# Kernel optimization log

Measured on AMD Instinct MI355X. Metric: run time of the kernel, lower is better.

## Reference

```python
import jax, jax.numpy as jnp
import numpy as np

# GPT-2 decoder (mlm=False path of the Keras GPT module), no past/KV-cache,
# no explicit mask -> causal mask, dropout disabled (training=False).
N_HEAD = 12
NINF = -10000.0  # Attention.ninf
EPS = 1e-6


def layer_norm(x, g, b):
    m = jnp.mean(x, axis=-1, keepdims=True)
    v = jnp.mean(jnp.square(x - m), axis=-1, keepdims=True)
    return (x - m) / jnp.sqrt(v + EPS) * g + b


def gelu(x):
    # 0.5*x*(1+erf(x/sqrt(2))) as in gelu_activating
    return 0.5 * x * (1.0 + jax.lax.erf(x * np.float32(1.0 / np.sqrt(2.0))))


def setup_inputs() -> dict:
    key = jax.random.key(0)
    B, S, D, L, V, CTX = 4, 512, 768, 12, 50257, 1024
    F = 4 * D
    ks = jax.random.split(key, 10)
    init = lambda k, shape: (jax.random.normal(k, shape, jnp.float32) * 0.02)
    return {
        "x": jax.random.randint(ks[0], (B, S), 0, V),
        "emb": init(ks[1], (V, D)),        # wte (tied output projection)
        "posemb": init(ks[2], (CTX, D)),   # wpe
        "ln1_g": jnp.ones((L, D)), "ln1_b": jnp.zeros((L, D)),
        "wqkv": init(ks[3], (L, D, 3 * D)), "bqkv": jnp.zeros((L, 3 * D)),
        "wo": init(ks[4], (L, D, D)), "bo": jnp.zeros((L, D)),
        "ln2_g": jnp.ones((L, D)), "ln2_b": jnp.zeros((L, D)),
        "wfc": init(ks[5], (L, D, F)), "bfc": jnp.zeros((L, F)),
        "wproj": init(ks[6], (L, F, D)), "bproj": jnp.zeros((L, D)),
        "lnf_g": jnp.ones((D,)), "lnf_b": jnp.zeros((D,)),
    }


def reference(x, emb, posemb, ln1_g, ln1_b, wqkv, bqkv, wo, bo,
              ln2_g, ln2_b, wfc, bfc, wproj, bproj, lnf_g, lnf_b):
    B, S = x.shape
    L, D, _ = wqkv.shape
    H = N_HEAD
    hd = D // H
    scale = np.float32(1.0 / np.sqrt(hd))

    # Embedding (mlm=False): token + positional, no layernorm
    h = emb[x] + posemb[:S]  # [B,S,D]

    # causal mask: positions j > i get NINF (m1 = range(q)[:,None] < range(k)-k+q)
    mask = (jnp.arange(S)[:, None] < jnp.arange(S)[None, :]).astype(jnp.float32) * NINF

    for i in range(L):
        # pre-norm attention
        qkv = layer_norm(h, ln1_g[i], ln1_b[i]) @ wqkv[i] + bqkv[i]  # [B,S,3D]
        q, k, v = jnp.split(qkv, 3, axis=-1)
        q = q.reshape(B, S, H, hd).transpose(0, 2, 1, 3)  # [B,H,S,hd]
        k = k.reshape(B, S, H, hd).transpose(0, 2, 1, 3)
        v = v.reshape(B, S, H, hd).transpose(0, 2, 1, 3)
        scores = jnp.einsum('bhqd,bhkd->bhqk', q, k) * scale + mask
        a = jax.nn.softmax(scores, axis=-1)  # [B,H,S,S]
        o = jnp.einsum('bhqk,bhkd->bhqd', a, v)
        o = o.transpose(0, 2, 1, 3).reshape(B, S, D)
        h = h + (o @ wo[i] + bo[i])  # residual
        # pre-norm MLP
        m = layer_norm(h, ln2_g[i], ln2_b[i])
        h = h + (gelu(m @ wfc[i] + bfc[i]) @ wproj[i] + bproj[i])

    hidden = layer_norm(h, lnf_g, lnf_b)          # model/lnorm_f
    logits = hidden @ emb.T                        # tied embedding projection
    probs = jax.nn.softmax(logits, axis=-1)        # softmax=True
    return (probs, hidden)
```

## Files before the change

### kernel.cpp

```cpp
#include <hip/hip_runtime.h>
#include <hip/hip_bf16.h>

typedef __bf16 bf16_t;
typedef bf16_t bf16x8 __attribute__((ext_vector_type(8)));
typedef float  f32x4  __attribute__((ext_vector_type(4)));

__device__ __forceinline__ void gload16(const void* g, void* l) {
    __builtin_amdgcn_global_load_lds(
        (const __attribute__((address_space(1))) unsigned int*)g,
        (__attribute__((address_space(3))) unsigned int*)l, 16, 0, 0);
}

__device__ __forceinline__ void drain_and_barrier() {
    __builtin_amdgcn_sched_barrier(0);
    asm volatile("s_waitcnt vmcnt(0)" ::: "memory");
    __builtin_amdgcn_s_barrier();
    __builtin_amdgcn_sched_barrier(0);
}

__global__ void embed_kernel(const int* __restrict__ x,
                             const float* __restrict__ emb,
                             const float* __restrict__ pos,
                             float* __restrict__ h,
                             int S, int D, int total)
{
    int i = blockIdx.x * blockDim.x + threadIdx.x;
    if (i >= total) return;
    int d  = i % D;
    int bs = i / D;
    int s  = bs % S;
    h[i] = emb[(long long)x[bs] * D + d] + pos[(long long)s * D + d];
}

__global__ void convert_bf16(const float* __restrict__ in, bf16_t* __restrict__ out, int n4)
{
    int i = blockIdx.x * blockDim.x + threadIdx.x;
    for (; i < n4; i += gridDim.x * blockDim.x) {
        float4 v = ((const float4*)in)[i];
        bf16_t* o = out + (size_t)i * 4;
        o[0] = (bf16_t)v.x; o[1] = (bf16_t)v.y; o[2] = (bf16_t)v.z; o[3] = (bf16_t)v.w;
    }
}

__global__ __launch_bounds__(256) void transpose_to_bf16(
    const float* __restrict__ in, bf16_t* __restrict__ out, int K, int N)
{
    const float* ip = in  + (size_t)blockIdx.z * K * N;
    bf16_t*      op = out + (size_t)blockIdx.z * K * N;
    __shared__ float t[32][33];
    const int n0 = blockIdx.x * 32, k0 = blockIdx.y * 32;
    const int tx = threadIdx.x, ty = threadIdx.y;
#pragma unroll
    for (int u = 0; u < 4; ++u)
        t[ty + u * 8][tx] = ip[(size_t)(k0 + ty + u * 8) * N + (n0 + tx)];
    __syncthreads();
#pragma unroll
    for (int u = 0; u < 4; ++u)
        op[(size_t)(n0 + ty + u * 8) * K + (k0 + tx)] = (bf16_t)t[tx][ty + u * 8];
}

__global__ __launch_bounds__(256) void layernorm_dual(
    const float* __restrict__ X, const float* __restrict__ g,
    const float* __restrict__ b, bf16_t* __restrict__ Yb,
    float* __restrict__ Yf, int D)
{
    const int row = blockIdx.x;
    const float* xr = X + (long long)row * D;
    const int tid = threadIdx.x;

    float vals[3];
    float s = 0.0f;
#pragma unroll
    for (int u = 0; u < 3; ++u) { vals[u] = xr[tid + u * 256]; s += vals[u]; }

    __shared__ float red[256];
    red[tid] = s;
    __syncthreads();
    for (int off = 128; off > 0; off >>= 1) {
        if (tid < off) red[tid] += red[tid + off];
        __syncthreads();
    }
    const float mean = red[0] / (float)D;
    __syncthreads();

    float vs = 0.0f;
#pragma unroll
    for (int u = 0; u < 3; ++u) { float d = vals[u] - mean; vs += d * d; }
    red[tid] = vs;
    __syncthreads();
    for (int off = 128; off > 0; off >>= 1) {
        if (tid < off) red[tid] += red[tid + off];
        __syncthreads();
    }
    const float var  = red[0] / (float)D;
    const float rstd = rsqrtf(var + 1e-6f);

#pragma unroll
    for (int u = 0; u < 3; ++u) {
        const int c = tid + u * 256;
        const float y = (vals[u] - mean) * rstd * g[c] + b[c];
        Yb[(long long)row * D + c] = (bf16_t)y;
        if (Yf) Yf[(long long)row * D + c] = y;
    }
}

__global__ __launch_bounds__(256) void flash_attn(
    const bf16_t* __restrict__ qkv, bf16_t* __restrict__ o)
{
    constexpr int S = 512, TD = 2304, D = 768, H = 12;
    const int qt = blockIdx.x;
    const int z  = blockIdx.y;
    const int bb = z / H, hh = z - bb * H;
    const int tid = threadIdx.x, lane = tid & 63, w = tid >> 6;
    const int fr = lane & 15, g = lane >> 4, sub = g * 8;

    __shared__ bf16_t kS[2][4096];
    __shared__ bf16_t vS[2][4096];
    __shared__ bf16_t pS[4][32 * 72];

    bf16x8 qf[2][2];
    const bf16_t* qbase = qkv + (size_t)(bb * S + qt * 128 + w * 32) * TD + hh * 64;
#pragma unroll
    for (int m = 0; m < 2; ++m)
#pragma unroll
        for (int ks = 0; ks < 2; ++ks) {
            bf16x8 v = *(const bf16x8*)&qbase[(size_t)(m * 16 + fr) * TD + ks * 32 + sub];
#pragma unroll
            for (int j = 0; j < 8; ++j) v[j] = v[j] * (bf16_t)0.125f;
            qf[m][ks] = v;
        }

    f32x4 oacc[2][4];
    float mrun[2][4], lrun[2][4];
#pragma unroll
    for (int m = 0; m < 2; ++m)
#pragma unroll
        for (int r = 0; r < 4; ++r) { mrun[m][r] = -3.0e38f; lrun[m][r] = 0.0f; }
#pragma unroll
    for (int m = 0; m < 2; ++m)
#pragma unroll
        for (int n = 0; n < 4; ++n)
            oacc[m][n] = (f32x4){0.f, 0.f, 0.f, 0.f};

    int qr[2][4];
#pragma unroll
    for (int m = 0; m < 2; ++m)
#pragma unroll
        for (int r = 0; r < 4; ++r)
            qr[m][r] = qt * 128 + w * 32 + m * 16 + g * 4 + r;

    const int srow8  = lane >> 3;
    const int schunk = (lane & 7) ^ (srow8 & 7);

    const bf16_t* kGbase = qkv + (size_t)(bb * S) * TD + D + hh * 64;
    const bf16_t* vGbase = qkv + (size_t)(bb * S) * TD + 2 * D + hh * 64;
    const int nkv = 2 * qt + 2;

    bf16x8 vreg[2];

#define STAGE_ISSUE(buf, t)                                                     \
    {                                                                           \
        _Pragma("unroll")                                                       \
        for (int it = 0; it < 2; ++it) {                                        \
            const int row = it * 32 + w * 8 + srow8;                            \
            gload16(kGbase + (size_t)((t) * 64 + row) * TD + schunk * 8,        \
                    &kS[buf][it * 2048 + w * 512]);                             \
        }                                                                       \
        _Pragma("unroll")                                                       \
        for (int it = 0; it < 2; ++it) {                                        \
            const int dch = w * 2 + it;                                         \
            vreg[it] = *(const bf16x8*)&vGbase[(size_t)((t) * 64 + lane) * TD + dch * 8]; \
        }                                                                       \
    }
#define STAGE_WRITE(buf)                                                        \
    {                                                                           \
        _Pragma("unroll")                                                       \
        for (int it = 0; it < 2; ++it) {                                        \
            const int dch = w * 2 + it;                                         \
            _Pragma("unroll")                                                   \
            for (int j = 0; j < 8; ++j) {                                       \
                const int d = dch * 8 + j;                                      \
                vS[buf][d * 64 + (((lane >> 3) ^ j) << 3) + (lane & 7)] = vreg[it][j]; \
            }                                                                   \
        }                                                                       \
    }

    STAGE_ISSUE(0, 0);
    STAGE_WRITE(0);
    __syncthreads();

    int cur = 0;
    for (int t = 0; t < nkv; ++t) {
        if (t + 1 < nkv) STAGE_ISSUE(cur ^ 1, t + 1);

        f32x4 sacc[2][4];
#pragma unroll
        for (int m = 0; m < 2; ++m)
#pragma unroll
            for (int n = 0; n < 4; ++n)
                sacc[m][n] = (f32x4){0.f, 0.f, 0.f, 0.f};
#pragma unroll
        for (int ks = 0; ks < 2; ++ks) {
            bf16x8 bK[4];
#pragma unroll
            for (int n = 0; n < 4; ++n) {
                const int rw = n * 16 + fr;
                const int c  = ks * 4 + g;
                bK[n] = *(const bf16x8*)&kS[cur][rw * 64 + ((c ^ (rw & 7)) << 3)];
            }
#pragma unroll
            for (int m = 0; m < 2; ++m)
#pragma unroll
                for (int n = 0; n < 4; ++n)
                    sacc[m][n] = __builtin_amdgcn_mfma_f32_16x16x32_bf16(
                        qf[m][ks], bK[n], sacc[m][n], 0, 0, 0);
        }

        if (t >= 2 * qt) {
#pragma unroll
            for (int m = 0; m < 2; ++m)
#pragma unroll
                for (int n = 0; n < 4; ++n) {
                    const int key = t * 64 + n * 16 + fr;
#pragma unroll
                    for (int r = 0; r < 4; ++r)
                        if (key > qr[m][r]) sacc[m][n][r] = -3.0e38f;
                }
        }

        float sf[2][4], rs[2][4];
#pragma unroll
        for (int m = 0; m < 2; ++m)
#pragma unroll
            for (int r = 0; r < 4; ++r) {
                float v = fmaxf(fmaxf(sacc[m][0][r], sacc[m][1][r]),
                                fmaxf(sacc[m][2][r], sacc[m][3][r]));
#pragma unroll
                for (int off = 1; off < 16; off <<= 1)
                    v = fmaxf(v, __shfl_xor(v, off));
                const float mn = fmaxf(mrun[m][r], v);
                sf[m][r] = __expf(mrun[m][r] - mn);
                mrun[m][r] = mn;
                lrun[m][r] *= sf[m][r];
            }
#pragma unroll
        for (int m = 0; m < 2; ++m)
#pragma unroll
            for (int n = 0; n < 4; ++n)
#pragma unroll
                for (int r = 0; r < 4; ++r)
                    oacc[m][n][r] *= sf[m][r];
#pragma unroll
        for (int m = 0; m < 2; ++m)
#pragma unroll
            for (int r = 0; r < 4; ++r) rs[m][r] = 0.0f;
#pragma unroll
        for (int m = 0; m < 2; ++m)
#pragma unroll
            for (int n = 0; n < 4; ++n)
#pragma unroll
                for (int r = 0; r < 4; ++r) {
                    const float p = __expf(sacc[m][n][r] - mrun[m][r]);
                    sacc[m][n][r] = p;
                    rs[m][r] += p;
                }
#pragma unroll
        for (int m = 0; m < 2; ++m)
#pragma unroll
            for (int r = 0; r < 4; ++r) {
                float v = rs[m][r];
#pragma unroll
                for (int off = 1; off < 16; off <<= 1) v += __shfl_xor(v, off);
                lrun[m][r] += v;
            }

        bf16_t* pw = pS[w];
#pragma unroll
        for (int m = 0; m < 2; ++m)
#pragma unroll
            for (int n = 0; n < 4; ++n)
#pragma unroll
                for (int r = 0; r < 4; ++r)
                    pw[(m * 16 + g * 4 + r) * 72 + n * 16 + fr] = (bf16_t)sacc[m][n][r];

#pragma unroll
        for (int ks = 0; ks < 2; ++ks) {
            bf16x8 pa[2], vb[4];
#pragma unroll
            for (int m = 0; m < 2; ++m)
                pa[m] = *(const bf16x8*)&pw[(m * 16 + fr) * 72 + ks * 32 + sub];
#pragma unroll
            for (int n = 0; n < 4; ++n) {
                const int rw = n * 16 + fr;
                const int c  = ks * 4 + g;
                vb[n] = *(const bf16x8*)&vS[cur][rw * 64 + ((c ^ (rw & 7)) << 3)];
            }
#pragma unroll
            for (int m = 0; m < 2; ++m)
#pragma unroll
                for (int n = 0; n < 4; ++n)
                    oacc[m][n] = __builtin_amdgcn_mfma_f32_16x16x32_bf16(
                        pa[m], vb[n], oacc[m][n], 0, 0, 0);
        }

        if (t + 1 < nkv) STAGE_WRITE(cur ^ 1);
        __syncthreads();
        cur ^= 1;
    }
#undef STAGE_ISSUE
#undef STAGE_WRITE

    bf16_t* obase = o + (size_t)(bb * S + qt * 128 + w * 32) * D + hh * 64;
#pragma unroll
    for (int m = 0; m < 2; ++m)
#pragma unroll
        for (int r = 0; r < 4; ++r) {
            const float inv = 1.0f / lrun[m][r];
#pragma unroll
            for (int n = 0; n < 4; ++n)
                obase[(size_t)(m * 16 + g * 4 + r) * D + n * 16 + fr] =
                    (bf16_t)(oacc[m][n][r] * inv);
        }
}

__global__ __launch_bounds__(256) void softmax_vocab(
    const bf16_t* __restrict__ logits, float* __restrict__ probs, int V, int Vp)
{
    const int tid = threadIdx.x;
    const bf16_t* lr = logits + (size_t)blockIdx.x * Vp;
    float* pr = probs + (size_t)blockIdx.x * V;
    const int n8 = V >> 3;

    float m = -3.0e38f, s = 0.0f;
    for (int c8 = tid; c8 < n8; c8 += 256) {
        const bf16x8 v = *(const bf16x8*)(lr + (size_t)c8 * 8);
        float f[8], lm = -3.0e38f;
#pragma unroll
        for (int j = 0; j < 8; ++j) { f[j] = (float)v[j]; lm = fmaxf(lm, f[j]); }
        if (lm > m) { s *= __expf(m - lm); m = lm; }
#pragma unroll
        for (int j = 0; j < 8; ++j) s += __expf(f[j] - m);
    }
    for (int c = n8 * 8 + tid; c < V; c += 256) {
        const float f = (float)lr[c];
        if (f > m) { s *= __expf(m - f); m = f; }
        s += __expf(f - m);
    }

    __shared__ float mS[256], sS[256];
    mS[tid] = m; sS[tid] = s;
    __syncthreads();
    for (int off = 128; off > 0; off >>= 1) {
        if (tid < off) {
            const float m1 = mS[tid], m2 = mS[tid + off];
            const float M_ = fmaxf(m1, m2);
            sS[tid] = sS[tid] * __expf(m1 - M_) + sS[tid + off] * __expf(m2 - M_);
            mS[tid] = M_;
        }
        __syncthreads();
    }
    const float M_  = mS[0];
    const float inv = 1.0f / sS[0];

    for (int c8 = tid; c8 < n8; c8 += 256) {
        const bf16x8 v = *(const bf16x8*)(lr + (size_t)c8 * 8);
#pragma unroll
        for (int j = 0; j < 8; ++j)
            pr[(size_t)c8 * 8 + j] = __expf((float)v[j] - M_) * inv;
    }
    for (int c = n8 * 8 + tid; c < V; c += 256)
        pr[c] = __expf((float)lr[c] - M_) * inv;
}

template<bool ADD, bool GELU_, bool OUTBF, bool DB, bool HALFN>
__device__ __forceinline__ void gemm_body(
    const bf16_t* __restrict__ A, const bf16_t* __restrict__ Bw,
    const float* __restrict__ bias, void* __restrict__ Cv,
    int M, int N, int K, int lda, int ldb, int ldc)
{
    constexpr int BN  = HALFN ? 64 : 128;
    constexpr int BUF = HALFN ? 12288 : 16384;
    __shared__ bf16_t lds[(DB ? 2 : 1) * BUF];

    const int tid  = threadIdx.x;
    const int lane = tid & 63;
    const int w    = tid >> 6;
    const int row0 = blockIdx.x * 128;
    const int col0 = blockIdx.y * BN;

    const int row8 = lane >> 3;
    const int sch  = (lane & 7) ^ row8;
    const int fr   = lane & 15;
    const int g    = lane >> 4;

    const int aRowB = row0 + w * 32;
    const int bRowB = HALFN ? (col0 + w * 16) : (col0 + w * 32);

    constexpr int MR = HALFN ? 2 : 4;
    const int wr = HALFN ? w : (w >> 1);
    const int wc = HALFN ? 0 : (w & 1);

    f32x4 acc[MR][4];
#pragma unroll
    for (int m = 0; m < MR; ++m)
#pragma unroll
        for (int n = 0; n < 4; ++n)
            acc[m][n] = (f32x4){0.f, 0.f, 0.f, 0.f};

    auto STAGE = [&](int buf, int k0) {
        bf16_t* lb = lds + buf * BUF;
#pragma unroll
        for (int it = 0; it < 4; ++it) {
            const int ar = aRowB + it * 8 + row8;
            gload16(A + (size_t)ar * lda + k0 + sch * 8, lb + w * 2048 + it * 512);
        }
#pragma unroll
        for (int it = 0; it < (HALFN ? 2 : 4); ++it) {
            int br = bRowB + it * 8 + row8;
            if (br >= N) br = 0;
            gload16(Bw + (size_t)br * ldb + k0 + sch * 8,
                    lb + 8192 + w * (HALFN ? 1024 : 2048) + it * 512);
        }
    };

    auto COMPUTE = [&](int buf) {
        bf16_t* lb = lds + buf * BUF;
#pragma unroll
        for (int ks = 0; ks < 2; ++ks) {
            bf16x8 af[MR], bfr[4];
            const int cs = ks * 4 + g;
#pragma unroll
            for (int m = 0; m < MR; ++m) {
                const int row = (HALFN ? w * 32 : wr * 64) + m * 16 + fr;
                af[m] = *(const bf16x8*)&lb[row * 64 + ((cs ^ (fr & 7)) << 3)];
            }
#pragma unroll
            for (int n = 0; n < 4; ++n) {
                const int row = (HALFN ? 0 : wc * 64) + n * 16 + fr;
                bfr[n] = *(const bf16x8*)&lb[8192 + row * 64 + ((cs ^ (fr & 7)) << 3)];
            }
#pragma unroll
            for (int m = 0; m < MR; ++m)
#pragma unroll
                for (int n = 0; n < 4; ++n)
                    acc[m][n] = __builtin_amdgcn_mfma_f32_16x16x32_bf16(
                        af[m], bfr[n], acc[m][n], 0, 0, 0);
        }
    };

    const int nt = K >> 6;
    if (DB) {
        STAGE(0, 0);
        drain_and_barrier();
        int cur = 0;
        for (int t = 0; t < nt; ++t) {
            if (t + 1 < nt) STAGE(cur ^ 1, (t + 1) << 6);
            COMPUTE(cur);
            drain_and_barrier();
            cur ^= 1;
        }
    } else {
        for (int t = 0; t < nt; ++t) {
            STAGE(0, t << 6);
            __syncthreads();
            COMPUTE(0);
            __syncthreads();
        }
    }

    const int rBase = row0 + (HALFN ? w * 32 : wr * 64) + g * 4;
    const int cBase = col0 + (HALFN ? 0 : wc * 64) + fr;
    float bv[4];
#pragma unroll
    for (int n = 0; n < 4; ++n) {
        const int c = cBase + n * 16;
        bv[n] = (bias && c < N) ? bias[c] : 0.0f;
    }
#pragma unroll
    for (int m = 0; m < MR; ++m) {
#pragma unroll
        for (int r = 0; r < 4; ++r) {
            const int rr = rBase + m * 16 + r;
#pragma unroll
            for (int n = 0; n < 4; ++n) {
                const int c = cBase + n * 16;
                if (c >= N) continue;
                float v = acc[m][n][r] + bv[n];
                if (GELU_) v = 0.5f * v * (1.0f + erff(v * 0.70710678118654752f));
                if (OUTBF) {
                    ((bf16_t*)Cv)[(size_t)rr * ldc + c] = (bf16_t)v;
                } else {
                    float* Cf = (float*)Cv;
                    const size_t idx = (size_t)rr * ldc + c;
                    if (ADD) v += Cf[idx];
                    Cf[idx] = v;
                }
            }
        }
    }
}

__global__ __launch_bounds__(256) void k_gemm_qkv(
    const bf16_t* A, const bf16_t* B, const float* bias, void* C,
    int M, int N, int K, int lda, int ldb, int ldc)
{ gemm_body<false, false, true, true, true>(A, B, bias, C, M, N, K, lda, ldb, ldc); }

__global__ __launch_bounds__(256) void k_gemm_oproj(
    const bf16_t* A, const bf16_t* B, const float* bias, void* C,
    int M, int N, int K, int lda, int ldb, int ldc)
{ gemm_body<true, false, false, true, true>(A, B, bias, C, M, N, K, lda, ldb, ldc); }

__global__ __launch_bounds__(256) void k_gemm_fc(
    const bf16_t* A, const bf16_t* B, const float* bias, void* C,
    int M, int N, int K, int lda, int ldb, int ldc)
{ gemm_body<false, true, true, true, true>(A, B, bias, C, M, N, K, lda, ldb, ldc); }

__global__ __launch_bounds__(256) void k_gemm_proj(
    const bf16_t* A, const bf16_t* B, const float* bias, void* C,
    int M, int N, int K, int lda, int ldb, int ldc)
{ gemm_body<true, false, false, true, true>(A, B, bias, C, M, N, K, lda, ldb, ldc); }

__global__ __launch_bounds__(256) void k_gemm_head(
    const bf16_t* __restrict__ A, const bf16_t* __restrict__ Bw,
    bf16_t* __restrict__ C, int M, int N, int K, int lda, int ldb, int ldc)
{
    __shared__ bf16_t lds[16384];

    const int tid  = threadIdx.x;
    const int lane = tid & 63;
    const int w    = tid >> 6;
    const int wr   = w >> 1, wc = w & 1;
    const int row0 = blockIdx.x * 128;
    const int col0 = blockIdx.y * 128;

    const int row8 = lane >> 3;
    const int sch  = (lane & 7) ^ row8;
    const int fr   = lane & 15;
    const int g    = lane >> 4;

    const int aRowB = row0 + w * 32;
    const int bRowB = col0 + w * 32;

    f32x4 acc[4][4];
#pragma unroll
    for (int m = 0; m < 4; ++m)
#pragma unroll
        for (int n = 0; n < 4; ++n)
            acc[m][n] = (f32x4){0.f, 0.f, 0.f, 0.f};

    for (int k0 = 0; k0 < K; k0 += 64) {
#pragma unroll
        for (int it = 0; it < 4; ++it) {
            const int ar = aRowB + it * 8 + row8;
            gload16(A + (size_t)ar * lda + k0 + sch * 8,
                    lds + w * 2048 + it * 512);
            int br = bRowB + it * 8 + row8;
            if (br >= N) br = 0;
            gload16(Bw + (size_t)br * ldb + k0 + sch * 8,
                    lds + 8192 + w * 2048 + it * 512);
        }
        __syncthreads();

#pragma unroll
        for (int ks = 0; ks < 2; ++ks) {
            bf16x8 af[4], bfr[4];
            const int cs = ks * 4 + g;
#pragma unroll
            for (int m = 0; m < 4; ++m) {
                const int row = wr * 64 + m * 16 + fr;
                af[m] = *(const bf16x8*)&lds[row * 64 + ((cs ^ (fr & 7)) << 3)];
            }
#pragma unroll
            for (int n = 0; n < 4; ++n) {
                const int row = wc * 64 + n * 16 + fr;
                bfr[n] = *(const bf16x8*)&lds[8192 + row * 64 + ((cs ^ (fr & 7)) << 3)];
            }
#pragma unroll
            for (int m = 0; m < 4; ++m)
#pragma unroll
                for (int n = 0; n < 4; ++n)
                    acc[m][n] = __builtin_amdgcn_mfma_f32_16x16x32_bf16(
                        af[m], bfr[n], acc[m][n], 0, 0, 0);
        }
        __syncthreads();
    }

    const int rBase = row0 + wr * 64 + g * 4;
    const int cBase = col0 + wc * 64 + fr;
#pragma unroll
    for (int n = 0; n < 4; ++n) {
        const int c = cBase + n * 16;
        if (c >= N) continue;
#pragma unroll
        for (int m = 0; m < 4; ++m)
#pragma unroll
            for (int r = 0; r < 4; ++r)
                C[(size_t)(rBase + m * 16 + r) * ldc + c] = (bf16_t)acc[m][n][r];
    }
}

extern "C" void kernel_launch(void* const* d_in, const int* in_sizes, int n_in,
                              void* d_out, int out_size, void* d_ws, size_t ws_size,
                              hipStream_t stream)
{
    constexpr int B = 4, S = 512, D = 768, L = 12, V = 50257, H = 12, F = 3072;
    constexpr int M  = B * S;
    constexpr int TD = 3 * D;
    constexpr int BH = B * H;
    constexpr int Vp = 50264;

    const int*   x    = (const int*)  d_in[0];
    const float* emb  = (const float*)d_in[1];
    const float* pos  = (const float*)d_in[2];
    const float* ln1g = (const float*)d_in[3];
    const float* ln1b = (const float*)d_in[4];
    const float* wqkv = (const float*)d_in[5];
    const float* bqkv = (const float*)d_in[6];
    const float* wo   = (const float*)d_in[7];
    const float* bo   = (const float*)d_in[8];
    const float* ln2g = (const float*)d_in[9];
    const float* ln2b = (const float*)d_in[10];
    const float* wfc  = (const float*)d_in[11];
    const float* bfc  = (const float*)d_in[12];
    const float* wpr  = (const float*)d_in[13];
    const float* bpr  = (const float*)d_in[14];
    const float* lnfg = (const float*)d_in[15];
    const float* lnfb = (const float*)d_in[16];

    float* probs  = (float*)d_out;
    float* hidden = probs + (size_t)M * V;

    float*  h      = (float*)d_ws;
    bf16_t* qkv_bf = (bf16_t*)(h + (size_t)M * D);
    bf16_t* xn_bf  = qkv_bf + (size_t)M * TD;
    bf16_t* o_bf   = xn_bf  + (size_t)M * D;
    bf16_t* mid_bf = o_bf   + (size_t)M * D;
    bf16_t* wqkvT  = mid_bf + (size_t)M * F;
    bf16_t* woT    = wqkvT  + (size_t)L * D * TD;
    bf16_t* wfcT   = woT    + (size_t)L * D * D;
    bf16_t* wprT   = wfcT   + (size_t)L * D * F;
    bf16_t* hid_bf = wprT   + (size_t)L * F * D;
    bf16_t* embB   = hid_bf + (size_t)M * D;
    bf16_t* logits = (bf16_t*)d_ws;

    convert_bf16<<<2048, 256, 0, stream>>>(emb, embB, (V * D) / 4);
    transpose_to_bf16<<<dim3(TD / 32, D / 32, L), dim3(32, 8), 0, stream>>>(wqkv, wqkvT, D, TD);
    transpose_to_bf16<<<dim3(D / 32,  D / 32, L), dim3(32, 8), 0, stream>>>(wo,   woT,   D, D);
    transpose_to_bf16<<<dim3(F / 32,  D / 32, L), dim3(32, 8), 0, stream>>>(wfc,  wfcT,  D, F);
    transpose_to_bf16<<<dim3(D / 32,  F / 32, L), dim3(32, 8), 0, stream>>>(wpr,  wprT,  F, D);

    embed_kernel<<<dim3((M * D + 255) / 256), 256, 0, stream>>>(x, emb, pos, h, S, D, M * D);

    for (int i = 0; i < L; ++i) {
        layernorm_dual<<<M, 256, 0, stream>>>(h, ln1g + (size_t)i * D, ln1b + (size_t)i * D,
                                              xn_bf, nullptr, D);

        k_gemm_qkv<<<dim3(M / 128, TD / 64), 256, 0, stream>>>(
            xn_bf, wqkvT + (size_t)i * D * TD, bqkv + (size_t)i * TD, qkv_bf,
            M, TD, D, D, D, TD);

        flash_attn<<<dim3(S / 128, BH), 256, 0, stream>>>(qkv_bf, o_bf);

        k_gemm_oproj<<<dim3(M / 128, D / 64), 256, 0, stream>>>(
            o_bf, woT + (size_t)i * D * D, bo + (size_t)i * D, h,
            M, D, D, D, D, D);

        layernorm_dual<<<M, 256, 0, stream>>>(h, ln2g + (size_t)i * D, ln2b + (size_t)i * D,
                                              xn_bf, nullptr, D);

        k_gemm_fc<<<dim3(M / 128, F / 64), 256, 0, stream>>>(
            xn_bf, wfcT + (size_t)i * D * F, bfc + (size_t)i * F, mid_bf,
            M, F, D, D, D, F);

        k_gemm_proj<<<dim3(M / 128, D / 64), 256, 0, stream>>>(
            mid_bf, wprT + (size_t)i * F * D, bpr + (size_t)i * D, h,
            M, D, F, F, F, D);
    }

    layernorm_dual<<<M, 256, 0, stream>>>(h, lnfg, lnfb, hid_bf, hidden, D);

    k_gemm_head<<<dim3(M / 128, (V + 127) / 128), 256, 0, stream>>>(
        hid_bf, embB, logits,
        M, V, D, D, D, Vp);

    softmax_vocab<<<M, 256, 0, stream>>>(logits, probs, V, Vp);
}
```

Baseline: 2.164 ms.

## Halve attention query tile and fuse softmax partial stats into head GEMM

Flash attention now uses 64-query tiles with 16 rows per wave, which doubles the grid and gives finer causal load balance. The LM-head GEMM epilogue now computes per-row partial max and sum-exp for each 128-column tile and writes them to workspace. The vocab softmax merges these partials instead of re-reading all logits in a first pass, which removes one full read of the large logits buffer. The workspace layout is also rebuilt so the logits alias the trunk buffers while the embedding copy and the partial statistics live in separate regions.

```diff
diff --git a/kernel.cpp b/kernel.cpp
--- a/kernel.cpp
+++ b/kernel.cpp
@@ -116,45 +116,35 @@
 
     __shared__ bf16_t kS[2][4096];
     __shared__ bf16_t vS[2][4096];
-    __shared__ bf16_t pS[4][32 * 72];
-
-    bf16x8 qf[2][2];
-    const bf16_t* qbase = qkv + (size_t)(bb * S + qt * 128 + w * 32) * TD + hh * 64;
-#pragma unroll
-    for (int m = 0; m < 2; ++m)
-#pragma unroll
-        for (int ks = 0; ks < 2; ++ks) {
-            bf16x8 v = *(const bf16x8*)&qbase[(size_t)(m * 16 + fr) * TD + ks * 32 + sub];
-#pragma unroll
-            for (int j = 0; j < 8; ++j) v[j] = v[j] * (bf16_t)0.125f;
-            qf[m][ks] = v;
-        }
-
-    f32x4 oacc[2][4];
-    float mrun[2][4], lrun[2][4];
-#pragma unroll
-    for (int m = 0; m < 2; ++m)
-#pragma unroll
-        for (int r = 0; r < 4; ++r) { mrun[m][r] = -3.0e38f; lrun[m][r] = 0.0f; }
-#pragma unroll
-    for (int m = 0; m < 2; ++m)
-#pragma unroll
-        for (int n = 0; n < 4; ++n)
-            oacc[m][n] = (f32x4){0.f, 0.f, 0.f, 0.f};
-
-    int qr[2][4];
-#pragma unroll
-    for (int m = 0; m < 2; ++m)
-#pragma unroll
-        for (int r = 0; r < 4; ++r)
-            qr[m][r] = qt * 128 + w * 32 + m * 16 + g * 4 + r;
+    __shared__ bf16_t pS[4][16 * 72];
+
+    bf16x8 qf[2];
+    const bf16_t* qbase = qkv + (size_t)(bb * S + qt * 64 + w * 16) * TD + hh * 64;
+#pragma unroll
+    for (int ks = 0; ks < 2; ++ks) {
+        bf16x8 v = *(const bf16x8*)&qbase[(size_t)fr * TD + ks * 32 + sub];
+#pragma unroll
+        for (int j = 0; j < 8; ++j) v[j] = v[j] * (bf16_t)0.125f;
+        qf[ks] = v;
+    }
+
+    f32x4 oacc[4];
+    float mrun[4], lrun[4];
+#pragma unroll
+    for (int r = 0; r < 4; ++r) { mrun[r] = -3.0e38f; lrun[r] = 0.0f; }
+#pragma unroll
+    for (int n = 0; n < 4; ++n) oacc[n] = (f32x4){0.f, 0.f, 0.f, 0.f};
+
+    int qr[4];
+#pragma unroll
+    for (int r = 0; r < 4; ++r) qr[r] = qt * 64 + w * 16 + g * 4 + r;
 
     const int srow8  = lane >> 3;
     const int schunk = (lane & 7) ^ (srow8 & 7);
 
     const bf16_t* kGbase = qkv + (size_t)(bb * S) * TD + D + hh * 64;
     const bf16_t* vGbase = qkv + (size_t)(bb * S) * TD + 2 * D + hh * 64;
-    const int nkv = 2 * qt + 2;
+    const int nkv = qt + 1;
 
     bf16x8 vreg[2];
 
@@ -193,12 +183,9 @@
     for (int t = 0; t < nkv; ++t) {
         if (t + 1 < nkv) STAGE_ISSUE(cur ^ 1, t + 1);
 
-        f32x4 sacc[2][4];
-#pragma unroll
-        for (int m = 0; m < 2; ++m)
-#pragma unroll
-            for (int n = 0; n < 4; ++n)
-                sacc[m][n] = (f32x4){0.f, 0.f, 0.f, 0.f};
+        f32x4 sacc[4];
+#pragma unroll
+        for (int n = 0; n < 4; ++n) sacc[n] = (f32x4){0.f, 0.f, 0.f, 0.f};
 #pragma unroll
         for (int ks = 0; ks < 2; ++ks) {
             bf16x8 bK[4];
@@ -209,86 +196,68 @@
                 bK[n] = *(const bf16x8*)&kS[cur][rw * 64 + ((c ^ (rw & 7)) << 3)];
             }
 #pragma unroll
-            for (int m = 0; m < 2; ++m)
-#pragma unroll
-                for (int n = 0; n < 4; ++n)
-                    sacc[m][n] = __builtin_amdgcn_mfma_f32_16x16x32_bf16(
-                        qf[m][ks], bK[n], sacc[m][n], 0, 0, 0);
-        }
-
-        if (t >= 2 * qt) {
-#pragma unroll
-            for (int m = 0; m < 2; ++m)
-#pragma unroll
-                for (int n = 0; n < 4; ++n) {
-                    const int key = t * 64 + n * 16 + fr;
-#pragma unroll
-                    for (int r = 0; r < 4; ++r)
-                        if (key > qr[m][r]) sacc[m][n][r] = -3.0e38f;
-                }
-        }
-
-        float sf[2][4], rs[2][4];
-#pragma unroll
-        for (int m = 0; m < 2; ++m)
+            for (int n = 0; n < 4; ++n)
+                sacc[n] = __builtin_amdgcn_mfma_f32_16x16x32_bf16(
+                    qf[ks], bK[n], sacc[n], 0, 0, 0);
+        }
+
+        if (t == qt) {
+#pragma unroll
+            for (int n = 0; n < 4; ++n) {
+                const int key = t * 64 + n * 16 + fr;
+#pragma unroll
+                for (int r = 0; r < 4; ++r)
+                    if (key > qr[r]) sacc[n][r] = -3.0e38f;
+            }
+        }
+
+        float sf[4], rs[4];
+#pragma unroll
+        for (int r = 0; r < 4; ++r) {
+            float v = fmaxf(fmaxf(sacc[0][r], sacc[1][r]),
+                            fmaxf(sacc[2][r], sacc[3][r]));
+#pragma unroll
+            for (int off = 1; off < 16; off <<= 1)
+                v = fmaxf(v, __shfl_xor(v, off));
+            const float mn = fmaxf(mrun[r], v);
+            sf[r] = __expf(mrun[r] - mn);
+            mrun[r] = mn;
+            lrun[r] *= sf[r];
+        }
+#pragma unroll
+        for (int n = 0; n < 4; ++n)
+#pragma unroll
+            for (int r = 0; r < 4; ++r)
+                oacc[n][r] *= sf[r];
+#pragma unroll
+        for (int r = 0; r < 4; ++r) rs[r] = 0.0f;
+#pragma unroll
+        for (int n = 0; n < 4; ++n)
 #pragma unroll
             for (int r = 0; r < 4; ++r) {
-                float v = fmaxf(fmaxf(sacc[m][0][r], sacc[m][1][r]),
-                                fmaxf(sacc[m][2][r], sacc[m][3][r]));
-#pragma unroll
-                for (int off = 1; off < 16; off <<= 1)
-                    v = fmaxf(v, __shfl_xor(v, off));
-                const float mn = fmaxf(mrun[m][r], v);
-                sf[m][r] = __expf(mrun[m][r] - mn);
-                mrun[m][r] = mn;
-                lrun[m][r] *= sf[m][r];
-            }
-#pragma unroll
-        for (int m = 0; m < 2; ++m)
-#pragma unroll
-            for (int n = 0; n < 4; ++n)
-#pragma unroll
-                for (int r = 0; r < 4; ++r)
-                    oacc[m][n][r] *= sf[m][r];
-#pragma unroll
-        for (int m = 0; m < 2; ++m)
-#pragma unroll
-            for (int r = 0; r < 4; ++r) rs[m][r] = 0.0f;
-#pragma unroll
-        for (int m = 0; m < 2; ++m)
-#pragma unroll
-            for (int n = 0; n < 4; ++n)
-#pragma unroll
-                for (int r = 0; r < 4; ++r) {
-                    const float p = __expf(sacc[m][n][r] - mrun[m][r]);
-                    sacc[m][n][r] = p;
-                    rs[m][r] += p;
-                }
-#pragma unroll
-        for (int m = 0; m < 2; ++m)
-#pragma unroll
-            for (int r = 0; r < 4; ++r) {
-                float v = rs[m][r];
-#pragma unroll
-                for (int off = 1; off < 16; off <<= 1) v += __shfl_xor(v, off);
-                lrun[m][r] += v;
-            }
+                const float p = __expf(sacc[n][r] - mrun[r]);
+                sacc[n][r] = p;
+                rs[r] += p;
+            }
+#pragma unroll
+        for (int r = 0; r < 4; ++r) {
+            float v = rs[r];
+#pragma unroll
+            for (int off = 1; off < 16; off <<= 1) v += __shfl_xor(v, off);
+            lrun[r] += v;
+        }
 
         bf16_t* pw = pS[w];
 #pragma unroll
-        for (int m = 0; m < 2; ++m)
-#pragma unroll
-            for (int n = 0; n < 4; ++n)
-#pragma unroll
-                for (int r = 0; r < 4; ++r)
-                    pw[(m * 16 + g * 4 + r) * 72 + n * 16 + fr] = (bf16_t)sacc[m][n][r];
+        for (int n = 0; n < 4; ++n)
+#pragma unroll
+            for (int r = 0; r < 4; ++r)
+                pw[(g * 4 + r) * 72 + n * 16 + fr] = (bf16_t)sacc[n][r];
 
 #pragma unroll
         for (int ks = 0; ks < 2; ++ks) {
-            bf16x8 pa[2], vb[4];
-#pragma unroll
-            for (int m = 0; m < 2; ++m)
-                pa[m] = *(const bf16x8*)&pw[(m * 16 + fr) * 72 + ks * 32 + sub];
+            bf16x8 pa, vb[4];
+            pa = *(const bf16x8*)&pw[fr * 72 + ks * 32 + sub];
 #pragma unroll
             for (int n = 0; n < 4; ++n) {
                 const int rw = n * 16 + fr;
@@ -296,11 +265,9 @@
                 vb[n] = *(const bf16x8*)&vS[cur][rw * 64 + ((c ^ (rw & 7)) << 3)];
             }
 #pragma unroll
-            for (int m = 0; m < 2; ++m)
-#pragma unroll
-                for (int n = 0; n < 4; ++n)
-                    oacc[m][n] = __builtin_amdgcn_mfma_f32_16x16x32_bf16(
-                        pa[m], vb[n], oacc[m][n], 0, 0, 0);
+            for (int n = 0; n < 4; ++n)
+                oacc[n] = __builtin_amdgcn_mfma_f32_16x16x32_bf16(
+                    pa, vb[n], oacc[n], 0, 0, 0);
         }
 
         if (t + 1 < nkv) STAGE_WRITE(cur ^ 1);
@@ -310,41 +277,35 @@
 #undef STAGE_ISSUE
 #undef STAGE_WRITE
 
-    bf16_t* obase = o + (size_t)(bb * S + qt * 128 + w * 32) * D + hh * 64;
-#pragma unroll
-    for (int m = 0; m < 2; ++m)
-#pragma unroll
-        for (int r = 0; r < 4; ++r) {
-            const float inv = 1.0f / lrun[m][r];
-#pragma unroll
-            for (int n = 0; n < 4; ++n)
-                obase[(size_t)(m * 16 + g * 4 + r) * D + n * 16 + fr] =
-                    (bf16_t)(oacc[m][n][r] * inv);
-        }
+    bf16_t* obase = o + (size_t)(bb * S + qt * 64 + w * 16) * D + hh * 64;
+#pragma unroll
+    for (int r = 0; r < 4; ++r) {
+        const float inv = 1.0f / lrun[r];
+#pragma unroll
+        for (int n = 0; n < 4; ++n)
+            obase[(size_t)(g * 4 + r) * D + n * 16 + fr] =
+                (bf16_t)(oacc[n][r] * inv);
+    }
 }
 
 __global__ __launch_bounds__(256) void softmax_vocab(
-    const bf16_t* __restrict__ logits, float* __restrict__ probs, int V, int Vp)
+    const bf16_t* __restrict__ logits, const float* __restrict__ pmax,
+    const float* __restrict__ psum, float* __restrict__ probs,
+    int V, int Vp, int NP)
 {
     const int tid = threadIdx.x;
-    const bf16_t* lr = logits + (size_t)blockIdx.x * Vp;
-    float* pr = probs + (size_t)blockIdx.x * V;
-    const int n8 = V >> 3;
+    const int row = blockIdx.x;
+    const bf16_t* lr = logits + (size_t)row * Vp;
+    float* pr = probs + (size_t)row * V;
+    const float* pm = pmax + (size_t)row * 400;
+    const float* ps = psum + (size_t)row * 400;
 
     float m = -3.0e38f, s = 0.0f;
-    for (int c8 = tid; c8 < n8; c8 += 256) {
-        const bf16x8 v = *(const bf16x8*)(lr + (size_t)c8 * 8);
-        float f[8], lm = -3.0e38f;
-#pragma unroll
-        for (int j = 0; j < 8; ++j) { f[j] = (float)v[j]; lm = fmaxf(lm, f[j]); }
-        if (lm > m) { s *= __expf(m - lm); m = lm; }
-#pragma unroll
-        for (int j = 0; j < 8; ++j) s += __expf(f[j] - m);
-    }
-    for (int c = n8 * 8 + tid; c < V; c += 256) {
-        const float f = (float)lr[c];
-        if (f > m) { s *= __expf(m - f); m = f; }
-        s += __expf(f - m);
+    for (int p = tid; p < NP; p += 256) {
+        const float om = pm[p], os = ps[p];
+        const float M_ = fmaxf(m, om);
+        s = s * __expf(m - M_) + os * __expf(om - M_);
+        m = M_;
     }
 
     __shared__ float mS[256], sS[256];
@@ -362,6 +323,7 @@
     const float M_  = mS[0];
     const float inv = 1.0f / sS[0];
 
+    const int n8 = V >> 3;
     for (int c8 = tid; c8 < n8; c8 += 256) {
         const bf16x8 v = *(const bf16x8*)(lr + (size_t)c8 * 8);
 #pragma unroll
@@ -522,7 +484,8 @@
 
 __global__ __launch_bounds__(256) void k_gemm_head(
     const bf16_t* __restrict__ A, const bf16_t* __restrict__ Bw,
-    bf16_t* __restrict__ C, int M, int N, int K, int lda, int ldb, int ldc)
+    bf16_t* __restrict__ C, float* __restrict__ pmax, float* __restrict__ psum,
+    int M, int N, int K, int lda, int ldb, int ldc)
 {
     __shared__ bf16_t lds[16384];
 
@@ -597,6 +560,50 @@
             for (int r = 0; r < 4; ++r)
                 C[(size_t)(rBase + m * 16 + r) * ldc + c] = (bf16_t)acc[m][n][r];
     }
+
+    float* sred = (float*)lds;
+#pragma unroll
+    for (int m = 0; m < 4; ++m) {
+#pragma unroll
+        for (int r = 0; r < 4; ++r) {
+            float lm = -3.0e38f;
+#pragma unroll
+            for (int n = 0; n < 4; ++n) {
+                const int c = cBase + n * 16;
+                if (c < N) lm = fmaxf(lm, (float)(bf16_t)acc[m][n][r]);
+            }
+            float ls = 0.0f;
+#pragma unroll
+            for (int n = 0; n < 4; ++n) {
+                const int c = cBase + n * 16;
+                if (c < N) ls += __expf((float)(bf16_t)acc[m][n][r] - lm);
+            }
+#pragma unroll
+            for (int off = 1; off < 16; off <<= 1) {
+                const float om = __shfl_xor(lm, off);
+                const float os = __shfl_xor(ls, off);
+                const float M_ = fmaxf(lm, om);
+                ls = ls * __expf(lm - M_) + os * __expf(om - M_);
+                lm = M_;
+            }
+            if (fr == 0) {
+                const int rl = wr * 64 + m * 16 + g * 4 + r;
+                sred[wc * 128 + rl] = lm;
+                sred[256 + wc * 128 + rl] = ls;
+            }
+        }
+    }
+    __syncthreads();
+    if ((w & 1) == 0) {
+        const int rl = (w >> 1) * 64 + lane;
+        const float m0 = sred[rl],       m1 = sred[128 + rl];
+        const float s0 = sred[256 + rl], s1 = sred[384 + rl];
+        const float M_ = fmaxf(m0, m1);
+        const float S_ = s0 * __expf(m0 - M_) + s1 * __expf(m1 - M_);
+        const size_t grow = row0 + rl;
+        pmax[grow * 400 + blockIdx.y] = M_;
+        psum[grow * 400 + blockIdx.y] = S_;
+    }
 }
 
 extern "C" void kernel_launch(void* const* d_in, const int* in_sizes, int n_in,
@@ -608,6 +615,7 @@
     constexpr int TD = 3 * D;
     constexpr int BH = B * H;
     constexpr int Vp = 50264;
+    constexpr int NP = (V + 127) / 128;
 
     const int*   x    = (const int*)  d_in[0];
     const float* emb  = (const float*)d_in[1];
@@ -630,18 +638,30 @@
     float* probs  = (float*)d_out;
     float* hidden = probs + (size_t)M * V;
 
-    float*  h      = (float*)d_ws;
-    bf16_t* qkv_bf = (bf16_t*)(h + (size_t)M * D);
-    bf16_t* xn_bf  = qkv_bf + (size_t)M * TD;
-    bf16_t* o_bf   = xn_bf  + (size_t)M * D;
-    bf16_t* mid_bf = o_bf   + (size_t)M * D;
-    bf16_t* wqkvT  = mid_bf + (size_t)M * F;
-    bf16_t* woT    = wqkvT  + (size_t)L * D * TD;
-    bf16_t* wfcT   = woT    + (size_t)L * D * D;
-    bf16_t* wprT   = wfcT   + (size_t)L * D * F;
-    bf16_t* hid_bf = wprT   + (size_t)L * F * D;
-    bf16_t* embB   = hid_bf + (size_t)M * D;
-    bf16_t* logits = (bf16_t*)d_ws;
+    char* wsb = (char*)d_ws;
+    size_t off = 0;
+    auto alloc = [&](size_t bytes) -> char* {
+        char* p = wsb + off;
+        off += (bytes + 255) & ~(size_t)255;
+        return p;
+    };
+    bf16_t* hid_bf = (bf16_t*)alloc((size_t)M * D * 2);
+    bf16_t* embB   = (bf16_t*)alloc((size_t)V * D * 2);
+    const size_t trunk_start = off;
+    float*  h      = (float*) alloc((size_t)M * D * 4);
+    bf16_t* qkv_bf = (bf16_t*)alloc((size_t)M * TD * 2);
+    bf16_t* xn_bf  = (bf16_t*)alloc((size_t)M * D * 2);
+    bf16_t* o_bf   = (bf16_t*)alloc((size_t)M * D * 2);
+    bf16_t* mid_bf = (bf16_t*)alloc((size_t)M * F * 2);
+    bf16_t* wqkvT  = (bf16_t*)alloc((size_t)L * D * TD * 2);
+    bf16_t* woT    = (bf16_t*)alloc((size_t)L * D * D * 2);
+    bf16_t* wfcT   = (bf16_t*)alloc((size_t)L * D * F * 2);
+    bf16_t* wprT   = (bf16_t*)alloc((size_t)L * F * D * 2);
+    const size_t logits_bytes = (size_t)M * Vp * 2;
+    if (off < trunk_start + logits_bytes) off = trunk_start + logits_bytes;
+    bf16_t* logits = (bf16_t*)(wsb + trunk_start);
+    float* pmax = (float*)alloc((size_t)M * 400 * 4);
+    float* psum = (float*)alloc((size_t)M * 400 * 4);
 
     convert_bf16<<<2048, 256, 0, stream>>>(emb, embB, (V * D) / 4);
     transpose_to_bf16<<<dim3(TD / 32, D / 32, L), dim3(32, 8), 0, stream>>>(wqkv, wqkvT, D, TD);
@@ -659,7 +679,7 @@
             xn_bf, wqkvT + (size_t)i * D * TD, bqkv + (size_t)i * TD, qkv_bf,
             M, TD, D, D, D, TD);
 
-        flash_attn<<<dim3(S / 128, BH), 256, 0, stream>>>(qkv_bf, o_bf);
+        flash_attn<<<dim3(S / 64, BH), 256, 0, stream>>>(qkv_bf, o_bf);
 
         k_gemm_oproj<<<dim3(M / 128, D / 64), 256, 0, stream>>>(
             o_bf, woT + (size_t)i * D * D, bo + (size_t)i * D, h,
@@ -679,9 +699,9 @@
 
     layernorm_dual<<<M, 256, 0, stream>>>(h, lnfg, lnfb, hid_bf, hidden, D);
 
-    k_gemm_head<<<dim3(M / 128, (V + 127) / 128), 256, 0, stream>>>(
-        hid_bf, embB, logits,
+    k_gemm_head<<<dim3(M / 128, NP), 256, 0, stream>>>(
+        hid_bf, embB, logits, pmax, psum,
         M, V, D, D, D, Vp);
 
-    softmax_vocab<<<M, 256, 0, stream>>>(logits, probs, V, Vp);
-}
+    softmax_vocab<<<M, 256, 0, stream>>>(logits, pmax, psum, probs, V, Vp, NP);
+}
```

Measured after the change: 2.164 ms. About the same (-0.0%).
